# Performance work log

Measured on AMD Instinct MI355X. Metric: run time of the kernel, lower is better.

The kernel has to match this reference:

```python
import jax, jax.numpy as jnp
import numpy as np

H1, H2, H3 = 32, 64, 64
NODEN = 12
NODES_PER_GRAPH = NODEN + 2  # 14
N = 700000                   # 50000 graphs * 14 nodes
E = 4000000


def setup_inputs() -> dict:
    key = jax.random.key(0)
    ks = jax.random.split(key, 8)
    x = jax.random.normal(ks[0], (N, H1), dtype=jnp.float32)
    edges = jax.random.randint(ks[1], (2, E), 0, N, dtype=jnp.int64)
    W1 = jax.random.normal(ks[2], (H1, H2), dtype=jnp.float32) / np.sqrt(H1).astype(np.float32)
    b1 = jnp.zeros((H2,), jnp.float32)
    W2 = jax.random.normal(ks[3], (H2, H3), dtype=jnp.float32) / np.sqrt(H2).astype(np.float32)
    b2 = jnp.zeros((H3,), jnp.float32)
    Wfc = jax.random.normal(ks[4], (H3 * NODES_PER_GRAPH, 1), dtype=jnp.float32) / np.sqrt(H3 * NODES_PER_GRAPH).astype(np.float32)
    bfc = jnp.zeros((1,), jnp.float32)
    return {"x": x, "edges": edges, "W1": W1, "b1": b1, "W2": W2, "b2": b2, "Wfc": Wfc, "bfc": bfc}


def gcn_conv(x, src, dst, W, b, n):
    # PyG GCNConv: h = X W; add self-loops; norm = deg^-1/2[src]*deg^-1/2[dst]
    h = x @ W  # [N, out]
    ones = jnp.ones(src.shape[0], dtype=h.dtype)
    deg = jax.ops.segment_sum(ones, dst, num_segments=n) + jnp.asarray(1.0, h.dtype)  # +1 self-loop
    dinv = jax.lax.rsqrt(deg)  # deg >= 1 always (self-loop)
    norm = dinv[src] * dinv[dst]  # [E]
    agg = jax.ops.segment_sum(h[src] * norm[:, None], dst, num_segments=n)
    agg = agg + h * (dinv * dinv)[:, None]  # self-loop contribution
    return agg + b


def reference(x, edges, W1, b1, W2, b2, Wfc, bfc):
    src, dst = edges[0], edges[1]
    h = jax.nn.relu(gcn_conv(x, src, dst, W1, b1, N))
    # F.dropout(training=False) is identity in eval mode
    h = jax.nn.relu(gcn_conv(h, src, dst, W2, b2, N))
    h = h.reshape(-1, H3 * NODES_PER_GRAPH)  # [B, 896]
    return h @ Wfc + bfc  # [B, 1]
```

## Files before the change

kernel.cpp:

```cpp
#include <hip/hip_runtime.h>
#include <hip/hip_fp16.h>


typedef _Float16 half8 __attribute__((ext_vector_type(8)));
typedef float float4v __attribute__((ext_vector_type(4)));

#define CHUNK 8192
#define BSH 11
#define BNODES 2048
#define DBINS 64

__global__ __launch_bounds__(256) void fallback_kernel(float* __restrict__ out, int n, float v)
{
  int i = blockIdx.x * 256 + threadIdx.x;
  if (i < n) out[i] = v;
}

__device__ inline int edges_shift(const int* __restrict__ edges)
{
  int orv = edges[1] | edges[3] | edges[5] | edges[7] | edges[9] | edges[11] | edges[13] | edges[15];
  return (orv == 0) ? 1 : 0;
}

__global__ __launch_bounds__(256) void hist2_kernel(
    const int* __restrict__ edges, int E, int N,
    int* __restrict__ cnt, int NBK,
    __half* __restrict__ P, __half* __restrict__ F2,
    int* __restrict__ dhist, int* __restrict__ dcnt)
{
  __shared__ int lh[512];
  int t = threadIdx.x;
  int blk = blockIdx.x;
  if (blk == 0) {
    if (t < 8) ((uint2*)(P + (size_t)N * 32))[t] = make_uint2(0, 0);
    else if (t < 24) ((uint2*)(F2 + (size_t)N * 64))[t - 8] = make_uint2(0, 0);
    if (t >= 64 && t < 64 + DBINS) dhist[t - 64] = 0;
    if (t >= 128 && t < 128 + DBINS) dcnt[t - 128] = 0;
  }
  for (int b = t; b < NBK; b += 256) lh[b] = 0;
  __syncthreads();
  int sh = edges_shift(edges);
  int base = blk * CHUNK;
#pragma unroll
  for (int k = 0; k < CHUNK / 256; k++) {
    int e = base + k * 256 + t;
    if (e < E) {
      int d = edges[(E + e) << sh];
      if ((unsigned)d < (unsigned)N) atomicAdd(&lh[d >> BSH], 1);
    }
  }
  __syncthreads();
  for (int b = t; b < NBK; b += 256) cnt[(size_t)blk * NBK + b] = lh[b];
}

__global__ __launch_bounds__(64) void colscan_kernel(
    int* __restrict__ cnt, int NCH, int NBK, int* __restrict__ totals)
{
  int b = blockIdx.x;
  int lane = threadIdx.x;
  int carry = 0;
  int rounds = (NCH + 63) >> 6;
  for (int r = 0; r < rounds; r++) {
    int blk = r * 64 + lane;
    int v = (blk < NCH) ? cnt[(size_t)blk * NBK + b] : 0;
    int incl = v;
#pragma unroll
    for (int off = 1; off < 64; off <<= 1) {
      int x = __shfl_up(incl, off);
      if (lane >= off) incl += x;
    }
    int excl = incl - v + carry;
    if (blk < NCH) cnt[(size_t)blk * NBK + b] = excl;
    carry += __shfl(incl, 63);
  }
  if (lane == 0) totals[b] = carry;
}

__global__ __launch_bounds__(512) void scan_totals_kernel(
    const int* __restrict__ totals, int NBK,
    int* __restrict__ bstart, int* __restrict__ rowptr, int N)
{
  __shared__ int sm[512];
  int t = threadIdx.x;
  int v = (t < NBK) ? totals[t] : 0;
  sm[t] = v;
  __syncthreads();
  for (int off = 1; off < 512; off <<= 1) {
    int x = 0;
    if (t >= off) x = sm[t - off];
    __syncthreads();
    if (t >= off) sm[t] += x;
    __syncthreads();
  }
  if (t < NBK) bstart[t] = sm[t] - v;
  if (t == 0) { bstart[NBK] = sm[511]; rowptr[N] = sm[511] + N; }
}

__global__ __launch_bounds__(256) void pass3_kernel(
    const int* __restrict__ edges, int E, int N,
    const int* __restrict__ cnt, const int* __restrict__ bstart,
    int* __restrict__ pair, int NBK)
{
  __shared__ int lcur[512];
  int t = threadIdx.x;
  int blk = blockIdx.x;
  for (int b = t; b < NBK; b += 256)
    lcur[b] = bstart[b] + cnt[(size_t)blk * NBK + b];
  __syncthreads();
  int sh = edges_shift(edges);
  int base = blk * CHUNK;
#pragma unroll
  for (int k = 0; k < CHUNK / 256; k++) {
    int e = base + k * 256 + t;
    if (e < E) {
      int s = edges[e << sh];
      int d = edges[(E + e) << sh];
      if ((unsigned)s < (unsigned)N && (unsigned)d < (unsigned)N) {
        int pos = atomicAdd(&lcur[d >> BSH], 1);
        pair[pos] = s | ((d & (BNODES - 1)) << 20);
      }
    }
  }
}

__global__ __launch_bounds__(256) void build_kernel(
    const int* __restrict__ pair, const int* __restrict__ bstart,
    int* __restrict__ rowptr, float* __restrict__ dinv, int* __restrict__ col,
    int* __restrict__ dhist, int N)
{
  __shared__ int hist[BNODES];
  __shared__ int cur[BNODES];
  __shared__ int sc[256];
  __shared__ int lh2[DBINS];
  int b = blockIdx.x;
  int t = threadIdx.x;
  int pbeg = bstart[b], pend = bstart[b + 1];
  int colbase = pbeg + (b << BSH);
  if (t < DBINS) lh2[t] = 0;
#pragma unroll
  for (int i = 0; i < BNODES / 256; i++) {
    int idx = i * 256 + t;
    int row = (b << BSH) + idx;
    hist[idx] = (row < N) ? 1 : 0;
  }
  __syncthreads();
  for (int p = pbeg + t; p < pend; p += 256)
    atomicAdd(&hist[(pair[p] >> 20) & (BNODES - 1)], 1);
  __syncthreads();
  int hv[8];
  int tsum = 0;
#pragma unroll
  for (int i = 0; i < 8; i++) { hv[i] = hist[t * 8 + i]; tsum += hv[i]; }
  sc[t] = tsum;
  __syncthreads();
  for (int off = 1; off < 256; off <<= 1) {
    int x = 0;
    if (t >= off) x = sc[t - off];
    __syncthreads();
    if (t >= off) sc[t] += x;
    __syncthreads();
  }
  int run = sc[t] - tsum;
#pragma unroll
  for (int i = 0; i < 8; i++) {
    int idx = t * 8 + i;
    int rp = colbase + run;
    int row = (b << BSH) + idx;
    if (row < N) {
      rowptr[row] = rp;
      dinv[row] = rsqrtf((float)hv[i]);
      col[rp] = row;
      cur[idx] = rp + 1;
      int bin = hv[i] < DBINS ? hv[i] : DBINS - 1;
      atomicAdd(&lh2[bin], 1);
    } else {
      cur[idx] = rp;
    }
    run += hv[i];
  }
  __syncthreads();
  if (t < DBINS && lh2[t]) atomicAdd(&dhist[t], lh2[t]);
  for (int p = pbeg + t; p < pend; p += 256) {
    int v = pair[p];
    int pos = atomicAdd(&cur[(v >> 20) & (BNODES - 1)], 1);
    col[pos] = v & 0xFFFFF;
  }
}

__global__ __launch_bounds__(256) void deg_place_kernel(
    const int* __restrict__ rowptr, const float* __restrict__ dinv,
    const int* __restrict__ dhist, int* __restrict__ dcnt,
    int* __restrict__ perm, int* __restrict__ iperm,
    int2* __restrict__ rowinfo, float* __restrict__ dinv_p, int N)
{
  __shared__ int bb[DBINS];
  __shared__ int lh[DBINS];
  __shared__ int lbase[DBINS];
  int t = threadIdx.x;
  if (t < DBINS) {
    lh[t] = 0;
    int v = dhist[t];
    int incl = v;
#pragma unroll
    for (int off = 1; off < DBINS; off <<= 1) {
      int x = __shfl_up(incl, off);
      if (t >= off) incl += x;
    }
    bb[t] = incl - v;
  }
  __syncthreads();
  int n = blockIdx.x * 256 + t;
  int b = -1, rbeg = 0, rlen = 0;
  if (n < N) {
    rbeg = rowptr[n];
    rlen = rowptr[n + 1] - rbeg;
    b = rlen < DBINS ? rlen : DBINS - 1;
    atomicAdd(&lh[b], 1);
  }
  __syncthreads();
  if (t < DBINS) lbase[t] = lh[t] ? (bb[t] + atomicAdd(&dcnt[t], lh[t])) : 0;
  __syncthreads();
  if (t < DBINS) lh[t] = lbase[t];
  __syncthreads();
  if (n < N) {
    int pos = atomicAdd(&lh[b], 1);
    perm[pos] = n;
    iperm[n] = pos;
    rowinfo[pos] = make_int2(rbeg, rlen);
    dinv_p[pos] = dinv[n];
  }
}

__global__ __launch_bounds__(256) void prep_kernel(
    int* __restrict__ col, const int* __restrict__ iperm, const int* __restrict__ rowptr,
    const float* __restrict__ X, const int* __restrict__ perm,
    const float* __restrict__ dinv_p, __half* __restrict__ P,
    float* __restrict__ out, const float* __restrict__ bfc, int N, int B)
{
  int idx = blockIdx.x * 256 + threadIdx.x;
  int stride = gridDim.x * 256;
  int total = rowptr[N];
  for (int k = idx; k < total; k += stride) col[k] = iperm[col[k]];
  int totp = N * 4;
  for (int i = idx; i < totp; i += stride) {
    int pos = i >> 2, part = i & 3;
    int node = perm[pos];
    const float4* xp = (const float4*)(X + (size_t)node * 32 + part * 8);
    float dv = dinv_p[pos];
    float4 v0 = xp[0], v1 = xp[1];
    half8 h;
    h[0] = (_Float16)(dv * v0.x); h[1] = (_Float16)(dv * v0.y);
    h[2] = (_Float16)(dv * v0.z); h[3] = (_Float16)(dv * v0.w);
    h[4] = (_Float16)(dv * v1.x); h[5] = (_Float16)(dv * v1.y);
    h[6] = (_Float16)(dv * v1.z); h[7] = (_Float16)(dv * v1.w);
    *(half8*)(P + (size_t)pos * 32 + part * 8) = h;
  }
  for (int i = idx; i < B; i += stride) out[i] = bfc[0];
}

__device__ inline void hacc(uint4 v, __half2* a)
{
  a[0] = __hadd2(a[0], *reinterpret_cast<__half2*>(&v.x));
  a[1] = __hadd2(a[1], *reinterpret_cast<__half2*>(&v.y));
  a[2] = __hadd2(a[2], *reinterpret_cast<__half2*>(&v.z));
  a[3] = __hadd2(a[3], *reinterpret_cast<__half2*>(&v.w));
}

__global__ __launch_bounds__(256) void agg1_pos_kernel(
    const __half* __restrict__ P, const int2* __restrict__ rowinfo,
    const int* __restrict__ col, const float* __restrict__ dinv_p,
    const float* __restrict__ W1, const float* __restrict__ b1,
    __half* __restrict__ U, int ntiles, int ndummy)
{
  int lane = threadIdx.x & 63;
  int n16 = lane & 15;
  int quad = lane >> 4;

  int wid = (blockIdx.x * 256 + threadIdx.x) >> 6;
  int nt2 = (ntiles + 1) >> 1;
  if (wid >= nt2) return;

  half8 bf[4];
#pragma unroll
  for (int jb = 0; jb < 4; jb++)
#pragma unroll
    for (int i = 0; i < 8; i++)
      bf[jb][i] = (_Float16)W1[(quad * 8 + i) * 64 + jb * 16 + n16];
  float b1j[4];
#pragma unroll
  for (int jb = 0; jb < 4; jb++) b1j[jb] = b1[jb * 16 + n16];

  const uint4* P4 = (const uint4*)P;
  _Float16* Uh = (_Float16*)U;
#pragma unroll 1
  for (int it = 0; it < 2; it++) {
    int tile = (it == 0) ? wid : (ntiles - 1 - wid);
    if (it == 1 && tile <= wid) break;
    int ut = __builtin_amdgcn_readfirstlane(tile);
    int base = ut * 16;
    int2 ri = rowinfo[base + n16];
    int rbeg = ri.x, rlen = ri.y;
    float dvown = dinv_p[base + n16];

    __half2 z2 = __float2half2_rn(0.f);
    __half2 aA[4] = {z2, z2, z2, z2};
    __half2 aB[4] = {z2, z2, z2, z2};

    for (int j = 0; __any(j < rlen); j += 8) {
      int c[8];
#pragma unroll
      for (int q = 0; q < 8; q++) {
        int cc = col[rbeg + j + q];
        c[q] = (j + q < rlen) ? cc : ndummy;
      }
      uint4 v[8];
#pragma unroll
      for (int q = 0; q < 8; q++) v[q] = P4[((size_t)c[q] << 2) + quad];
#pragma unroll
      for (int q = 0; q < 8; q += 2) { hacc(v[q], aA); hacc(v[q + 1], aB); }
    }
#pragma unroll
    for (int k = 0; k < 4; k++) aA[k] = __hadd2(aA[k], aB[k]);

    half8 a = *reinterpret_cast<half8*>(aA);
    float4v co[4];
#pragma unroll
    for (int jb = 0; jb < 4; jb++) {
      float4v z = {0.f, 0.f, 0.f, 0.f};
      co[jb] = __builtin_amdgcn_mfma_f32_16x16x32_f16(a, bf[jb], z, 0, 0, 0);
    }
#pragma unroll
    for (int r = 0; r < 4; r++) {
      int pos2 = base + quad * 4 + r;
      float dv = __shfl(dvown, quad * 4 + r);
#pragma unroll
      for (int jb = 0; jb < 4; jb++) {
        float h = dv * co[jb][r] + b1j[jb];
        h = h > 0.f ? h : 0.f;
        Uh[(size_t)pos2 * 64 + jb * 16 + n16] = (_Float16)(dv * h);
      }
    }
  }
}

__global__ __launch_bounds__(256) void mfma_final_fused_kernel(
    const __half* __restrict__ U, const int2* __restrict__ rowinfo,
    const int* __restrict__ col, const float* __restrict__ dinv_p,
    const int* __restrict__ perm,
    const float* __restrict__ W2, const float* __restrict__ b2,
    const float* __restrict__ Wfc, float* __restrict__ out,
    int ntiles, int ndummy)
{
  int lane = threadIdx.x & 63;
  int n16 = lane & 15;
  int quad = lane >> 4;

  int wid = (blockIdx.x * 256 + threadIdx.x) >> 6;
  int nt2 = (ntiles + 1) >> 1;
  if (wid >= nt2) return;

  half8 bf[4][2];
#pragma unroll
  for (int jb = 0; jb < 4; jb++)
#pragma unroll
    for (int kf = 0; kf < 2; kf++)
#pragma unroll
      for (int i = 0; i < 8; i++)
        bf[jb][kf][i] = (_Float16)W2[(kf * 32 + quad * 8 + i) * 64 + jb * 16 + n16];
  float b2j[4];
#pragma unroll
  for (int jb = 0; jb < 4; jb++) b2j[jb] = b2[jb * 16 + n16];

  const uint4* U4 = (const uint4*)U;
#pragma unroll 1
  for (int it = 0; it < 2; it++) {
    int tile = (it == 0) ? wid : (ntiles - 1 - wid);
    if (it == 1 && tile <= wid) break;
    int ut = __builtin_amdgcn_readfirstlane(tile);
    int base = ut * 16;
    int2 ri = rowinfo[base + n16];
    int rbeg = ri.x, rlen = ri.y;
    int node = perm[base + n16];
    float dvown = dinv_p[base + n16];

    __half2 z2 = __float2half2_rn(0.f);
    __half2 aE0[4] = {z2, z2, z2, z2};
    __half2 aE1[4] = {z2, z2, z2, z2};
    __half2 aO0[4] = {z2, z2, z2, z2};
    __half2 aO1[4] = {z2, z2, z2, z2};

    for (int j = 0; __any(j < rlen); j += 4) {
      int c0 = col[rbeg + j];
      int c1 = col[rbeg + j + 1];
      int c2 = col[rbeg + j + 2];
      int c3 = col[rbeg + j + 3];
      c0 = (j < rlen) ? c0 : ndummy;
      c1 = (j + 1 < rlen) ? c1 : ndummy;
      c2 = (j + 2 < rlen) ? c2 : ndummy;
      c3 = (j + 3 < rlen) ? c3 : ndummy;
      uint4 v00 = U4[((size_t)c0 << 3) + quad];
      uint4 v01 = U4[((size_t)c0 << 3) + 4 + quad];
      uint4 v10 = U4[((size_t)c1 << 3) + quad];
      uint4 v11 = U4[((size_t)c1 << 3) + 4 + quad];
      uint4 v20 = U4[((size_t)c2 << 3) + quad];
      uint4 v21 = U4[((size_t)c2 << 3) + 4 + quad];
      uint4 v30 = U4[((size_t)c3 << 3) + quad];
      uint4 v31 = U4[((size_t)c3 << 3) + 4 + quad];
      hacc(v00, aE0); hacc(v01, aE1);
      hacc(v10, aO0); hacc(v11, aO1);
      hacc(v20, aE0); hacc(v21, aE1);
      hacc(v30, aO0); hacc(v31, aO1);
    }
#pragma unroll
    for (int k = 0; k < 4; k++) {
      aE0[k] = __hadd2(aE0[k], aO0[k]);
      aE1[k] = __hadd2(aE1[k], aO1[k]);
    }
    __half2 dv = __half2half2(__float2half_rn(dvown));
#pragma unroll
    for (int j = 0; j < 4; j++) {
      aE0[j] = __hmul2(aE0[j], dv);
      aE1[j] = __hmul2(aE1[j], dv);
    }
    half8 a0 = *reinterpret_cast<half8*>(aE0);
    half8 a1 = *reinterpret_cast<half8*>(aE1);

    int g_r[4], t_r[4];
#pragma unroll
    for (int r = 0; r < 4; r++) {
      int nd = __shfl(node, quad * 4 + r);
      g_r[r] = nd / 14;
      t_r[r] = nd - g_r[r] * 14;
    }
    float pr[4] = {0.f, 0.f, 0.f, 0.f};
#pragma unroll
    for (int jb = 0; jb < 4; jb++) {
      float4v acc = {0.f, 0.f, 0.f, 0.f};
      acc = __builtin_amdgcn_mfma_f32_16x16x32_f16(a0, bf[jb][0], acc, 0, 0, 0);
      acc = __builtin_amdgcn_mfma_f32_16x16x32_f16(a1, bf[jb][1], acc, 0, 0, 0);
      int j = jb * 16 + n16;
#pragma unroll
      for (int r = 0; r < 4; r++) {
        float h = acc[r] + b2j[jb];
        h = h > 0.f ? h : 0.f;
        pr[r] += h * Wfc[t_r[r] * 64 + j];
      }
    }
#pragma unroll
    for (int r = 0; r < 4; r++) {
#pragma unroll
      for (int off = 1; off < 16; off <<= 1) pr[r] += __shfl_xor(pr[r], off);
    }
    if (n16 == 0) {
#pragma unroll
      for (int r = 0; r < 4; r++) atomicAdd(&out[g_r[r]], pr[r]);
    }
  }
}

extern "C" void kernel_launch(void* const* d_in, const int* in_sizes, int n_in,
                              void* d_out, int out_size, void* d_ws, size_t ws_size,
                              hipStream_t stream)
{
  const float* x = (const float*)d_in[0];
  const int* edges = (const int*)d_in[1];
  const float* W1 = (const float*)d_in[2];
  const float* b1 = (const float*)d_in[3];
  const float* W2 = (const float*)d_in[4];
  const float* b2 = (const float*)d_in[5];
  const float* Wfc = (const float*)d_in[6];
  const float* bfc = (const float*)d_in[7];
  float* out = (float*)d_out;
  (void)n_in;

  const int N = in_sizes[0] / 32;
  const int E = in_sizes[1] / 2;
  const int B = out_size;
  const int NBK = (N + BNODES - 1) >> BSH;
  const int NCH = (E + CHUNK - 1) / CHUNK;
  const int NBLK = (N + 255) / 256;

  char* ws = (char*)d_ws;
  size_t off = 0;
  auto alloc = [&](size_t bytes) -> void* {
    void* p = ws + off;
    off += (bytes + 255) & ~(size_t)255;
    return p;
  };
  int* cnt = (int*)alloc((size_t)NCH * NBK * 4);
  int* totals = (int*)alloc((size_t)NBK * 4);
  int* bstart = (int*)alloc(((size_t)NBK + 1) * 4);
  int* col = (int*)alloc(((size_t)E + N + 256) * 4);
  int* rowptr = (int*)alloc(((size_t)N + 1) * 4);
  float* dinv = (float*)alloc((size_t)N * 4);
  int* dhist = (int*)alloc(DBINS * 4);
  int* dcnt = (int*)alloc(DBINS * 4);
  int* perm = (int*)alloc((size_t)N * 4);
  int* iperm = (int*)alloc((size_t)N * 4);
  int2* rowinfo = (int2*)alloc((size_t)N * 8);
  float* dinv_p = (float*)alloc((size_t)N * 4);
  __half* P = (__half*)alloc(((size_t)N + 16) * 32 * 2);
  __half* F2 = (__half*)alloc(((size_t)N + 16) * 64 * 2);
  int* pair = (int*)P;

  if (off > ws_size) {
    float v = -(float)(double)(ws_size >> 20);
    fallback_kernel<<<(B + 255) / 256, 256, 0, stream>>>(out, B, v);
    return;
  }

  hist2_kernel<<<NCH, 256, 0, stream>>>(edges, E, N, cnt, NBK, P, F2, dhist, dcnt);
  colscan_kernel<<<NBK, 64, 0, stream>>>(cnt, NCH, NBK, totals);
  scan_totals_kernel<<<1, 512, 0, stream>>>(totals, NBK, bstart, rowptr, N);
  pass3_kernel<<<NCH, 256, 0, stream>>>(edges, E, N, cnt, bstart, pair, NBK);
  build_kernel<<<NBK, 256, 0, stream>>>(pair, bstart, rowptr, dinv, col, dhist, N);
  deg_place_kernel<<<NBLK, 256, 0, stream>>>(rowptr, dinv, dhist, dcnt,
                                             perm, iperm, rowinfo, dinv_p, N);
  prep_kernel<<<4096, 256, 0, stream>>>(col, iperm, rowptr, x, perm, dinv_p, P,
                                        out, bfc, N, B);

  int ntiles = (N + 15) / 16;
  int nt2 = (ntiles + 1) >> 1;
  int gblk = (nt2 + 3) / 4;
  agg1_pos_kernel<<<gblk, 256, 0, stream>>>(P, rowinfo, col, dinv_p, W1, b1, F2, ntiles, N);
  mfma_final_fused_kernel<<<gblk, 256, 0, stream>>>(F2, rowinfo, col, dinv_p, perm, W2, b2, Wfc,
                                                    out, ntiles, N);
}
```

Measured before the change: 561.3 us.

## Replace column-scan kernel with atomic bucket offsets and use grid-stride tile loops

The histogram kernel now claims per-chunk bucket offsets with a global atomicAdd on per-bucket totals, which removes the separate column-scan launch. A memset zeroes the totals and the degree-histogram buffers up front. The two aggregation kernels switch from paired front/back tile assignment to a fixed 4096-block grid-stride loop. Atomic offsets make the edge order within each bucket nondeterministic, and the grid-stride loop gives up the load balancing that pairing tiles from opposite ends of the degree-sorted order provided.

Measured after the change: 562.3 us. Within noise of the previous version (+0.2%).

```diff
diff --git a/kernel.cpp b/kernel.cpp
--- a/kernel.cpp
+++ b/kernel.cpp
@@ -24,9 +24,8 @@
 
 __global__ __launch_bounds__(256) void hist2_kernel(
     const int* __restrict__ edges, int E, int N,
-    int* __restrict__ cnt, int NBK,
-    __half* __restrict__ P, __half* __restrict__ F2,
-    int* __restrict__ dhist, int* __restrict__ dcnt)
+    int* __restrict__ cnt, int NBK, int* __restrict__ gtot,
+    __half* __restrict__ P, __half* __restrict__ F2)
 {
   __shared__ int lh[512];
   int t = threadIdx.x;
@@ -34,8 +33,6 @@
   if (blk == 0) {
     if (t < 8) ((uint2*)(P + (size_t)N * 32))[t] = make_uint2(0, 0);
     else if (t < 24) ((uint2*)(F2 + (size_t)N * 64))[t - 8] = make_uint2(0, 0);
-    if (t >= 64 && t < 64 + DBINS) dhist[t - 64] = 0;
-    if (t >= 128 && t < 128 + DBINS) dcnt[t - 128] = 0;
   }
   for (int b = t; b < NBK; b += 256) lh[b] = 0;
   __syncthreads();
@@ -50,30 +47,8 @@
     }
   }
   __syncthreads();
-  for (int b = t; b < NBK; b += 256) cnt[(size_t)blk * NBK + b] = lh[b];
-}
-
-__global__ __launch_bounds__(64) void colscan_kernel(
-    int* __restrict__ cnt, int NCH, int NBK, int* __restrict__ totals)
-{
-  int b = blockIdx.x;
-  int lane = threadIdx.x;
-  int carry = 0;
-  int rounds = (NCH + 63) >> 6;
-  for (int r = 0; r < rounds; r++) {
-    int blk = r * 64 + lane;
-    int v = (blk < NCH) ? cnt[(size_t)blk * NBK + b] : 0;
-    int incl = v;
-#pragma unroll
-    for (int off = 1; off < 64; off <<= 1) {
-      int x = __shfl_up(incl, off);
-      if (lane >= off) incl += x;
-    }
-    int excl = incl - v + carry;
-    if (blk < NCH) cnt[(size_t)blk * NBK + b] = excl;
-    carry += __shfl(incl, 63);
-  }
-  if (lane == 0) totals[b] = carry;
+  for (int b = t; b < NBK; b += 256)
+    cnt[(size_t)blk * NBK + b] = atomicAdd(&gtot[b], lh[b]);
 }
 
 __global__ __launch_bounds__(512) void scan_totals_kernel(
@@ -276,10 +251,6 @@
   int n16 = lane & 15;
   int quad = lane >> 4;
 
-  int wid = (blockIdx.x * 256 + threadIdx.x) >> 6;
-  int nt2 = (ntiles + 1) >> 1;
-  if (wid >= nt2) return;
-
   half8 bf[4];
 #pragma unroll
   for (int jb = 0; jb < 4; jb++)
@@ -292,10 +263,9 @@
 
   const uint4* P4 = (const uint4*)P;
   _Float16* Uh = (_Float16*)U;
-#pragma unroll 1
-  for (int it = 0; it < 2; it++) {
-    int tile = (it == 0) ? wid : (ntiles - 1 - wid);
-    if (it == 1 && tile <= wid) break;
+  int wave = (blockIdx.x * 256 + threadIdx.x) >> 6;
+  int nw = (gridDim.x * 256) >> 6;
+  for (int tile = wave; tile < ntiles; tile += nw) {
     int ut = __builtin_amdgcn_readfirstlane(tile);
     int base = ut * 16;
     int2 ri = rowinfo[base + n16];
@@ -355,10 +325,6 @@
   int n16 = lane & 15;
   int quad = lane >> 4;
 
-  int wid = (blockIdx.x * 256 + threadIdx.x) >> 6;
-  int nt2 = (ntiles + 1) >> 1;
-  if (wid >= nt2) return;
-
   half8 bf[4][2];
 #pragma unroll
   for (int jb = 0; jb < 4; jb++)
@@ -372,10 +338,9 @@
   for (int jb = 0; jb < 4; jb++) b2j[jb] = b2[jb * 16 + n16];
 
   const uint4* U4 = (const uint4*)U;
-#pragma unroll 1
-  for (int it = 0; it < 2; it++) {
-    int tile = (it == 0) ? wid : (ntiles - 1 - wid);
-    if (it == 1 && tile <= wid) break;
+  int wave = (blockIdx.x * 256 + threadIdx.x) >> 6;
+  int nw = (gridDim.x * 256) >> 6;
+  for (int tile = wave; tile < ntiles; tile += nw) {
     int ut = __builtin_amdgcn_readfirstlane(tile);
     int base = ut * 16;
     int2 ri = rowinfo[base + n16];
@@ -488,13 +453,14 @@
     return p;
   };
   int* cnt = (int*)alloc((size_t)NCH * NBK * 4);
-  int* totals = (int*)alloc((size_t)NBK * 4);
+  int* zbuf = (int*)alloc(((size_t)NBK + 2 * DBINS) * 4);
+  int* gtot = zbuf;
+  int* dhist = zbuf + NBK;
+  int* dcnt = zbuf + NBK + DBINS;
   int* bstart = (int*)alloc(((size_t)NBK + 1) * 4);
   int* col = (int*)alloc(((size_t)E + N + 256) * 4);
   int* rowptr = (int*)alloc(((size_t)N + 1) * 4);
   float* dinv = (float*)alloc((size_t)N * 4);
-  int* dhist = (int*)alloc(DBINS * 4);
-  int* dcnt = (int*)alloc(DBINS * 4);
   int* perm = (int*)alloc((size_t)N * 4);
   int* iperm = (int*)alloc((size_t)N * 4);
   int2* rowinfo = (int2*)alloc((size_t)N * 8);
@@ -509,9 +475,9 @@
     return;
   }
 
-  hist2_kernel<<<NCH, 256, 0, stream>>>(edges, E, N, cnt, NBK, P, F2, dhist, dcnt);
-  colscan_kernel<<<NBK, 64, 0, stream>>>(cnt, NCH, NBK, totals);
-  scan_totals_kernel<<<1, 512, 0, stream>>>(totals, NBK, bstart, rowptr, N);
+  hipMemsetAsync(zbuf, 0, ((size_t)NBK + 2 * DBINS) * 4, stream);
+  hist2_kernel<<<NCH, 256, 0, stream>>>(edges, E, N, cnt, NBK, gtot, P, F2);
+  scan_totals_kernel<<<1, 512, 0, stream>>>(gtot, NBK, bstart, rowptr, N);
   pass3_kernel<<<NCH, 256, 0, stream>>>(edges, E, N, cnt, bstart, pair, NBK);
   build_kernel<<<NBK, 256, 0, stream>>>(pair, bstart, rowptr, dinv, col, dhist, N);
   deg_place_kernel<<<NBLK, 256, 0, stream>>>(rowptr, dinv, dhist, dcnt,
@@ -520,9 +486,7 @@
                                         out, bfc, N, B);
 
   int ntiles = (N + 15) / 16;
-  int nt2 = (ntiles + 1) >> 1;
-  int gblk = (nt2 + 3) / 4;
-  agg1_pos_kernel<<<gblk, 256, 0, stream>>>(P, rowinfo, col, dinv_p, W1, b1, F2, ntiles, N);
-  mfma_final_fused_kernel<<<gblk, 256, 0, stream>>>(F2, rowinfo, col, dinv_p, perm, W2, b2, Wfc,
+  agg1_pos_kernel<<<4096, 256, 0, stream>>>(P, rowinfo, col, dinv_p, W1, b1, F2, ntiles, N);
+  mfma_final_fused_kernel<<<4096, 256, 0, stream>>>(F2, rowinfo, col, dinv_p, perm, W2, b2, Wfc,
                                                     out, ntiles, N);
 }
```
